# Kernel optimization log

Hardware: AMD Instinct MI355X
Metric: run time of the kernel (lower is better)

Reference implementation:

```python
import jax, jax.numpy as jnp
import numpy as np

N, E, D, H, G, C = 50000, 600000, 128, 128, 512, 1000
HP = H // 5  # attention-MLP bottleneck (hidden_dim // 5)


def setup_inputs() -> dict:
    key = jax.random.key(0)
    ks = jax.random.split(key, 18)
    cfg_nodes = jax.random.normal(ks[0], (N, D), jnp.float32)
    cfg_relations = jax.random.randint(ks[1], (2, E), 0, N, dtype=jnp.int32)
    pos = jnp.sort(jax.random.randint(ks[2], (G + 1,), 0, N, dtype=jnp.int32))
    node_pos = pos.at[0].set(0).at[-1].set(N)

    def lin(k, fi, fo):
        return jax.random.normal(k, (fi, fo), jnp.float32) / np.sqrt(fi)

    return dict(
        cfg_nodes=cfg_nodes, cfg_relations=cfg_relations, node_pos=node_pos,
        # GATConv layer 1 (in=D, out=H, heads=1)
        W_g1=lin(ks[3], D, H),
        att_src1=jax.random.normal(ks[4], (H,), jnp.float32) / np.sqrt(H),
        att_dst1=jax.random.normal(ks[5], (H,), jnp.float32) / np.sqrt(H),
        b_g1=jnp.zeros((H,), jnp.float32),
        # GATConv layer 2 (in=H, out=H, heads=1, concat=False)
        W_g2=lin(ks[6], H, H),
        att_src2=jax.random.normal(ks[7], (H,), jnp.float32) / np.sqrt(H),
        att_dst2=jax.random.normal(ks[8], (H,), jnp.float32) / np.sqrt(H),
        b_g2=jnp.zeros((H,), jnp.float32),
        # GraphLocalAttention projection MLP
        Wp1=lin(ks[9], H, HP), bp1=jnp.zeros((HP,), jnp.float32),
        Wp2=jax.random.normal(ks[10], (HP,), jnp.float32) / np.sqrt(HP),
        bp2=jnp.zeros((), jnp.float32),
        # final classifier
        Wl=lin(ks[11], H, C), bl=jnp.zeros((C,), jnp.float32),
    )


def _gat_conv(x, src, dst, W, a_src, a_dst, b, n_nodes):
    # PyG GATConv (heads=1): h = xW; e_ij = LeakyReLU(a_s.h_j + a_d.h_i);
    # alpha = softmax over incoming edges of each target; out_i = sum alpha*h_j + b
    h = x @ W                                    # [N, F]
    as_ = h @ a_src                              # [N]
    ad_ = h @ a_dst                              # [N]
    e = jax.nn.leaky_relu(as_[src] + ad_[dst], 0.2)   # [E]
    m = jax.ops.segment_max(e, dst, num_segments=n_nodes)
    ex = jnp.exp(e - m[dst])
    s = jax.ops.segment_sum(ex, dst, num_segments=n_nodes)
    alpha = ex / s[dst]
    out = jax.ops.segment_sum(alpha[:, None] * h[src], dst, num_segments=n_nodes)
    return out + b


def reference(cfg_nodes, cfg_relations, node_pos,
              W_g1, att_src1, att_dst1, b_g1,
              W_g2, att_src2, att_dst2, b_g2,
              Wp1, bp1, Wp2, bp2, Wl, bl):
    n = cfg_nodes.shape[0]
    # add self-loops (PyG GATConv default)
    loops = jnp.arange(n, dtype=cfg_relations.dtype)
    src = jnp.concatenate([cfg_relations[0], loops])
    dst = jnp.concatenate([cfg_relations[1], loops])
    # dropout layers are identity in eval mode
    x = _gat_conv(cfg_nodes, src, dst, W_g1, att_src1, att_dst1, b_g1, n)
    x = jax.nn.elu(x)
    x = _gat_conv(x, src, dst, W_g2, att_src2, att_dst2, b_g2, n)
    # ragged segment attention pooling (attn_by_batch, fully vectorized)
    energy = jax.nn.relu(x @ Wp1 + bp1) @ Wp2 + bp2          # [N]
    seg = jnp.clip(jnp.searchsorted(node_pos, jnp.arange(n), side='right') - 1, 0, G - 1)
    m = jax.ops.segment_max(energy, seg, num_segments=G)
    ex = jnp.exp(energy - m[seg])
    s = jax.ops.segment_sum(ex, seg, num_segments=G)
    w = ex / s[seg]                                           # per-segment softmax
    pooled = jax.ops.segment_sum(w[:, None] * x, seg, num_segments=G)  # [G, H]
    return pooled @ Wl + bl                                   # [G, C]
```

## Files before the change

kernel.cpp:

```cpp
#include <hip/hip_runtime.h>
#include <hip/hip_bf16.h>
#include <math.h>

#define WAVE 64
#define GR 32

typedef __attribute__((ext_vector_type(8))) _Float16 half8;
typedef __attribute__((ext_vector_type(4))) float f32x4;
typedef __attribute__((ext_vector_type(4))) _Float16 half4;

__global__ void count_pack(const int* __restrict__ dst, int* __restrict__ deg, int E, int nbC,
                           const float* __restrict__ W1, const float* __restrict__ W2,
                           _Float16* __restrict__ W1h, _Float16* __restrict__ W2h,
                           const float* __restrict__ Wp1, int HP,
                           _Float16* __restrict__ Ph) {
    int b = blockIdx.x;
    if (b < nbC) {
        int e = (b * 256 + threadIdx.x) * 2;
        if (e + 1 < E) {
            int2 d = *(const int2*)(dst + e);
            atomicAdd(&deg[d.x], 1);
            atomicAdd(&deg[d.y], 1);
        } else if (e < E) {
            atomicAdd(&deg[dst[e]], 1);
        }
    } else if (b < nbC + 128) {
        int pb = b - nbC;
        const float* W = (pb >= 64) ? W2 : W1;
        _Float16* Hf = (pb >= 64) ? W2h : W1h;
        int idx = (pb & 63) * 256 + threadIdx.x;
        int j = idx & 7;
        int lane = (idx >> 3) & 63;
        int kc = (idx >> 9) & 3;
        int nt = idx >> 11;
        int k = kc * 32 + (lane >> 4) * 8 + j;
        int ncol = nt * 16 + (lane & 15);
        Hf[idx] = (_Float16)W[k * 128 + ncol];
    } else {
        int idx = (b - nbC - 128) * 256 + threadIdx.x;
        int j = idx & 7;
        int lane = (idx >> 3) & 63;
        int kc = (idx >> 9) & 3;
        int nt = idx >> 11;
        int k = kc * 32 + (lane >> 4) * 8 + j;
        int ncol = nt * 16 + (lane & 15);
        float x = (ncol < HP) ? Wp1[k * HP + ncol] : 0.f;
        Ph[idx] = (_Float16)x;
    }
}

__global__ void scan_block(const int* __restrict__ in, int* __restrict__ part,
                           int* __restrict__ bsums, int n) {
    __shared__ int tmp[256];
    int tid = threadIdx.x;
    int i = blockIdx.x * 256 + tid;
    int v = (i < n) ? in[i] : 0;
    tmp[tid] = v;
    __syncthreads();
    for (int o = 1; o < 256; o <<= 1) {
        int t = (tid >= o) ? tmp[tid - o] : 0;
        __syncthreads();
        tmp[tid] += t;
        __syncthreads();
    }
    if (i < n) part[i] = tmp[tid] - v;
    if (tid == 255) bsums[blockIdx.x] = tmp[255];
}

__global__ void scan_finish(const int* __restrict__ part, const int* __restrict__ bsums,
                            int* __restrict__ offs, int* __restrict__ cursor,
                            int n, int Etot) {
    __shared__ int acc[256];
    int b = blockIdx.x, tid = threadIdx.x;
    int s = 0;
    for (int i = tid; i < b; i += 256) s += bsums[i];
    acc[tid] = s;
    __syncthreads();
    for (int o = 128; o > 0; o >>= 1) {
        if (tid < o) acc[tid] += acc[tid + o];
        __syncthreads();
    }
    int prefix = acc[0];
    int i = b * 256 + tid;
    if (i < n) {
        int v = part[i] + prefix;
        offs[i] = v;
        cursor[i] = v;
    }
    if (b == 0 && tid == 0) offs[n] = Etot;
}

__global__ void scatter_edges(const int* __restrict__ src, const int* __restrict__ dst,
                              int* __restrict__ cursor, int* __restrict__ csr_src,
                              int* __restrict__ csr_dst, int E) {
    int e = (blockIdx.x * 256 + threadIdx.x) * 2;
    if (e + 1 < E) {
        int2 d = *(const int2*)(dst + e);
        int2 s = *(const int2*)(src + e);
        int p0 = atomicAdd(&cursor[d.x], 1);
        csr_src[p0] = s.x;
        csr_dst[p0] = d.x;
        int p1 = atomicAdd(&cursor[d.y], 1);
        csr_src[p1] = s.y;
        csr_dst[p1] = d.y;
    } else if (e < E) {
        int p = atomicAdd(&cursor[dst[e]], 1);
        csr_src[p] = src[e];
        csr_dst[p] = dst[e];
    }
}

__global__ __launch_bounds__(256) void gemm_mfma(const float* __restrict__ X,
                                                 const _Float16* __restrict__ Bh,
                                                 const float* __restrict__ a_s,
                                                 const float* __restrict__ a_d,
                                                 _Float16* __restrict__ Hout,
                                                 float* __restrict__ as_,
                                                 float* __restrict__ ad_, int n) {
    __shared__ char lds[GR * 136 * 4];
    _Float16* Xh = (_Float16*)lds;
    float* Hs = (float*)lds;

    int tid = threadIdx.x;
    int base = blockIdx.x * GR;
    const float4* X4 = (const float4*)X;

#pragma unroll
    for (int i = 0; i < 4; ++i) {
        int idx = i * 256 + tid;
        int row = idx >> 5, c4 = idx & 31;
        int rs = base + row; if (rs >= n) rs = n - 1;
        float4 v = X4[(size_t)rs * 32 + c4];
        half4 hv = {(_Float16)v.x, (_Float16)v.y, (_Float16)v.z, (_Float16)v.w};
        *(half4*)(Xh + row * 136 + c4 * 4) = hv;
    }
    __syncthreads();

    int wid = tid >> 6, lane = tid & 63;
    int quad = lane >> 4, l16 = lane & 15;
    int rowA = (wid & 1) * 16 + l16;
    int ntb = (wid >> 1) * 4;

    f32x4 acc[4];
#pragma unroll
    for (int t = 0; t < 4; ++t) acc[t] = (f32x4){0.f, 0.f, 0.f, 0.f};

    for (int kc = 0; kc < 4; ++kc) {
        half8 Ah = *(const half8*)(Xh + rowA * 136 + kc * 32 + quad * 8);
#pragma unroll
        for (int nt = 0; nt < 4; ++nt) {
            half8 Bv = *(const half8*)(Bh + (((size_t)((ntb + nt) * 4 + kc)) * 64 + lane) * 8);
            acc[nt] = __builtin_amdgcn_mfma_f32_16x16x32_f16(Ah, Bv, acc[nt], 0, 0, 0);
        }
    }
    __syncthreads();

    int rowD0 = (wid & 1) * 16 + quad * 4;
#pragma unroll
    for (int nt = 0; nt < 4; ++nt)
#pragma unroll
        for (int r = 0; r < 4; ++r)
            Hs[(rowD0 + r) * 136 + (ntb + nt) * 16 + l16] = acc[nt][r];
    __syncthreads();

    const float4* Hs4 = (const float4*)Hs;
    half4* H4 = (half4*)Hout;
#pragma unroll
    for (int i = 0; i < 4; ++i) {
        int idx = i * 256 + tid;
        int row = idx >> 5, c4 = idx & 31;
        int grow = base + row;
        if (grow < n) {
            float4 v = Hs4[row * 34 + c4];
            half4 hv = {(_Float16)v.x, (_Float16)v.y, (_Float16)v.z, (_Float16)v.w};
            H4[(size_t)grow * 32 + c4] = hv;
        }
    }

    int drow = tid >> 3, q = tid & 7;
    const float4* as4 = (const float4*)a_s;
    const float4* ad4 = (const float4*)a_d;
    float s = 0.f, d = 0.f;
#pragma unroll
    for (int j = 0; j < 4; ++j) {
        float4 v = Hs4[drow * 34 + q * 4 + j];
        float4 a = as4[q * 4 + j];
        float4 b = ad4[q * 4 + j];
        s += v.x * a.x + v.y * a.y + v.z * a.z + v.w * a.w;
        d += v.x * b.x + v.y * b.y + v.z * b.z + v.w * b.w;
    }
    s += __shfl_xor(s, 1, WAVE); s += __shfl_xor(s, 2, WAVE); s += __shfl_xor(s, 4, WAVE);
    d += __shfl_xor(d, 1, WAVE); d += __shfl_xor(d, 2, WAVE); d += __shfl_xor(d, 4, WAVE);
    if (q == 0 && base + drow < n) {
        as_[base + drow] = s;
        ad_[base + drow] = d;
    }
}

__device__ __forceinline__ float leaky02(float x) { return x > 0.f ? x : 0.2f * x; }

__global__ __launch_bounds__(256) void edge_weights(const int* __restrict__ csr_src,
                                                    const int* __restrict__ csr_dst,
                                                    const float* __restrict__ as_,
                                                    const float* __restrict__ ad_,
                                                    int2* __restrict__ sw, int E) {
    int i = (blockIdx.x * 256 + threadIdx.x) * 4;
    if (i + 3 < E) {
        int4 s = *(const int4*)(csr_src + i);
        int4 d = *(const int4*)(csr_dst + i);
        float wx = __expf(leaky02(as_[s.x] + ad_[d.x]));
        float wy = __expf(leaky02(as_[s.y] + ad_[d.y]));
        float wz = __expf(leaky02(as_[s.z] + ad_[d.z]));
        float ww = __expf(leaky02(as_[s.w] + ad_[d.w]));
        int4 lo = make_int4(s.x, __float_as_int(wx), s.y, __float_as_int(wy));
        int4 hi = make_int4(s.z, __float_as_int(wz), s.w, __float_as_int(ww));
        *(int4*)(sw + i) = lo;
        *(int4*)(sw + i + 2) = hi;
    } else {
        for (; i < E; ++i) {
            float w = __expf(leaky02(as_[csr_src[i]] + ad_[csr_dst[i]]));
            sw[i] = make_int2(csr_src[i], __float_as_int(w));
        }
    }
}

__global__ __launch_bounds__(256) void gat_aggregate(const _Float16* __restrict__ h,
                                                     const int2* __restrict__ sw,
                                                     const float* __restrict__ as_,
                                                     const float* __restrict__ ad_,
                                                     const int* __restrict__ offs,
                                                     const float* __restrict__ bias,
                                                     float* __restrict__ out, int n, int act) {
    int node = blockIdx.x * 4 + (threadIdx.x >> 6);
    int lane = threadIdx.x & 63;
    if (node >= n) return;
    int beg = offs[node], end = offs[node + 1];
    int q4 = lane >> 4, l = lane & 15;
    const half8* h8 = (const half8*)h;

    float w_self = __expf(leaky02(as_[node] + ad_[node]));
    float facc[8];
    {
        half8 v = h8[(size_t)node * 16 + l];
        float ws = (q4 == 0) ? w_self : 0.f;
#pragma unroll
        for (int i = 0; i < 8; ++i) facc[i] = ws * (float)v[i];
    }
    float sacc = (lane == 0) ? w_self : 0.f;
#pragma unroll 2
    for (int j = beg; j < end; j += 4) {
        int j0 = j + q4;
        bool valid = j0 < end;
        int jc = valid ? j0 : (end - 1);
        int2 e = sw[jc];
        int s = valid ? e.x : node;
        float w = valid ? __int_as_float(e.y) : 0.f;
        half8 v = h8[(size_t)s * 16 + l];
#pragma unroll
        for (int i = 0; i < 8; ++i) facc[i] = fmaf(w, (float)v[i], facc[i]);
        sacc += (l == 0) ? w : 0.f;
    }
#pragma unroll
    for (int i = 0; i < 8; ++i) {
        facc[i] += __shfl_xor(facc[i], 16, WAVE);
        facc[i] += __shfl_xor(facc[i], 32, WAVE);
    }
    sacc += __shfl_xor(sacc, 16, WAVE);
    sacc += __shfl_xor(sacc, 32, WAVE);
    float inv_s = 1.f / __shfl(sacc, 0, WAVE);
    if (q4 == 0) {
        const float4* b4 = (const float4*)bias;
        float4 b0 = b4[l * 2], b1 = b4[l * 2 + 1];
        float4 o0, o1;
        o0.x = fmaf(facc[0], inv_s, b0.x);
        o0.y = fmaf(facc[1], inv_s, b0.y);
        o0.z = fmaf(facc[2], inv_s, b0.z);
        o0.w = fmaf(facc[3], inv_s, b0.w);
        o1.x = fmaf(facc[4], inv_s, b1.x);
        o1.y = fmaf(facc[5], inv_s, b1.y);
        o1.z = fmaf(facc[6], inv_s, b1.z);
        o1.w = fmaf(facc[7], inv_s, b1.w);
        if (act == 1) {
            o0.x = o0.x > 0.f ? o0.x : expm1f(o0.x);
            o0.y = o0.y > 0.f ? o0.y : expm1f(o0.y);
            o0.z = o0.z > 0.f ? o0.z : expm1f(o0.z);
            o0.w = o0.w > 0.f ? o0.w : expm1f(o0.w);
            o1.x = o1.x > 0.f ? o1.x : expm1f(o1.x);
            o1.y = o1.y > 0.f ? o1.y : expm1f(o1.y);
            o1.z = o1.z > 0.f ? o1.z : expm1f(o1.z);
            o1.w = o1.w > 0.f ? o1.w : expm1f(o1.w);
        }
        float4* o4 = (float4*)(out + (size_t)node * 128);
        o4[l * 2] = o0;
        o4[l * 2 + 1] = o1;
    }
}

__global__ __launch_bounds__(256) void energy_mfma(const float* __restrict__ X,
                                                   const _Float16* __restrict__ Ph,
                                                   const float* __restrict__ bp1,
                                                   const float* __restrict__ Wp2,
                                                   const float* __restrict__ bp2,
                                                   float* __restrict__ energy, int n, int HP) {
    __shared__ _Float16 Xh[GR * 136];
    int tid = threadIdx.x;
    int base = blockIdx.x * GR;
    const float4* X4 = (const float4*)X;
#pragma unroll
    for (int i = 0; i < 4; ++i) {
        int idx = i * 256 + tid;
        int row = idx >> 5, c4 = idx & 31;
        int rs = base + row; if (rs >= n) rs = n - 1;
        float4 v = X4[(size_t)rs * 32 + c4];
        half4 hv = {(_Float16)v.x, (_Float16)v.y, (_Float16)v.z, (_Float16)v.w};
        *(half4*)(Xh + row * 136 + c4 * 4) = hv;
    }
    __syncthreads();

    int wid = tid >> 6, lane = tid & 63;
    if (wid >= 2) return;
    int quad = lane >> 4, l16 = lane & 15;
    int rowA = wid * 16 + l16;

    f32x4 acc0 = (f32x4){0.f, 0.f, 0.f, 0.f};
    f32x4 acc1 = (f32x4){0.f, 0.f, 0.f, 0.f};
    for (int kc = 0; kc < 4; ++kc) {
        half8 Ah = *(const half8*)(Xh + rowA * 136 + kc * 32 + quad * 8);
        half8 B0 = *(const half8*)(Ph + (((size_t)kc) * 64 + lane) * 8);
        half8 B1 = *(const half8*)(Ph + (((size_t)(4 + kc)) * 64 + lane) * 8);
        acc0 = __builtin_amdgcn_mfma_f32_16x16x32_f16(Ah, B0, acc0, 0, 0, 0);
        acc1 = __builtin_amdgcn_mfma_f32_16x16x32_f16(Ah, B1, acc1, 0, 0, 0);
    }

    float b0 = bp1[l16];
    float w0 = Wp2[l16];
    int c1 = 16 + l16;
    int c1c = c1 < HP ? c1 : HP - 1;
    float b1 = bp1[c1c];
    float w1 = (c1 < HP) ? Wp2[c1c] : 0.f;
    float bp2v = bp2[0];
#pragma unroll
    for (int r = 0; r < 4; ++r) {
        float h0 = acc0[r] + b0;
        h0 = h0 > 0.f ? h0 : 0.f;
        float h1 = acc1[r] + b1;
        h1 = h1 > 0.f ? h1 : 0.f;
        float v = h0 * w0 + h1 * w1;
        v += __shfl_xor(v, 1, WAVE);
        v += __shfl_xor(v, 2, WAVE);
        v += __shfl_xor(v, 4, WAVE);
        v += __shfl_xor(v, 8, WAVE);
        int row = base + wid * 16 + quad * 4 + r;
        if (l16 == 0 && row < n) energy[row] = v + bp2v;
    }
}

__global__ __launch_bounds__(256) void seg_pool_classify(const float* __restrict__ X,
                                                         const float* __restrict__ energy,
                                                         const int* __restrict__ node_pos,
                                                         const float* __restrict__ Wl,
                                                         const float* __restrict__ bl,
                                                         float* __restrict__ out, int C) {
    int g = blockIdx.x;
    int beg = node_pos[g], end = node_pos[g + 1];
    int tid = threadIdx.x;
    __shared__ float sred[256];
    __shared__ float4 red[256];
    __shared__ float pP[128];

    float m = -INFINITY;
    for (int i = beg + tid; i < end; i += 256) m = fmaxf(m, energy[i]);
    sred[tid] = m;
    __syncthreads();
    for (int o = 128; o > 0; o >>= 1) {
        if (tid < o) sred[tid] = fmaxf(sred[tid], sred[tid + o]);
        __syncthreads();
    }
    m = sred[0];
    __syncthreads();
    float s = 0.f;
    for (int i = beg + tid; i < end; i += 256) s += __expf(energy[i] - m);
    sred[tid] = s;
    __syncthreads();
    for (int o = 128; o > 0; o >>= 1) {
        if (tid < o) sred[tid] += sred[tid + o];
        __syncthreads();
    }
    s = sred[0];
    __syncthreads();
    float inv = (end > beg && s > 0.f) ? 1.f / s : 0.f;

    int quad = tid & 31;
    int rg = tid >> 5;
    const float4* X4 = (const float4*)X;
    float4 acc = make_float4(0.f, 0.f, 0.f, 0.f);
    for (int i = beg + rg; i < end; i += 8) {
        float w = __expf(energy[i] - m) * inv;
        float4 v = X4[(size_t)i * 32 + quad];
        acc.x = fmaf(w, v.x, acc.x);
        acc.y = fmaf(w, v.y, acc.y);
        acc.z = fmaf(w, v.z, acc.z);
        acc.w = fmaf(w, v.w, acc.w);
    }
    red[tid] = acc;
    __syncthreads();
    if (rg < 4) {
        float4 o = red[tid + 128];
        acc.x += o.x; acc.y += o.y; acc.z += o.z; acc.w += o.w;
        red[tid] = acc;
    }
    __syncthreads();
    if (rg < 2) {
        float4 o = red[tid + 64];
        acc.x += o.x; acc.y += o.y; acc.z += o.z; acc.w += o.w;
        red[tid] = acc;
    }
    __syncthreads();
    if (rg == 0) {
        float4 o = red[tid + 32];
        acc.x += o.x; acc.y += o.y; acc.z += o.z; acc.w += o.w;
        pP[4 * quad + 0] = acc.x;
        pP[4 * quad + 1] = acc.y;
        pP[4 * quad + 2] = acc.z;
        pP[4 * quad + 3] = acc.w;
    }
    __syncthreads();

    for (int c = tid; c < C; c += 256) {
        float a = bl[c];
#pragma unroll 8
        for (int k = 0; k < 128; ++k) a = fmaf(pP[k], Wl[(size_t)k * C + c], a);
        out[(size_t)g * C + c] = a;
    }
}

extern "C" void kernel_launch(void* const* d_in, const int* in_sizes, int n_in,
                              void* d_out, int out_size, void* d_ws, size_t ws_size,
                              hipStream_t stream) {
    const float* cfg_nodes = (const float*)d_in[0];
    const int* rel = (const int*)d_in[1];
    const int* node_pos = (const int*)d_in[2];
    const float* W_g1 = (const float*)d_in[3];
    const float* att_src1 = (const float*)d_in[4];
    const float* att_dst1 = (const float*)d_in[5];
    const float* b_g1 = (const float*)d_in[6];
    const float* W_g2 = (const float*)d_in[7];
    const float* att_src2 = (const float*)d_in[8];
    const float* att_dst2 = (const float*)d_in[9];
    const float* b_g2 = (const float*)d_in[10];
    const float* Wp1 = (const float*)d_in[11];
    const float* bp1 = (const float*)d_in[12];
    const float* Wp2 = (const float*)d_in[13];
    const float* bp2 = (const float*)d_in[14];
    const float* Wl = (const float*)d_in[15];
    const float* bl = (const float*)d_in[16];

    const int N = in_sizes[0] / 128;
    const int E = in_sizes[1] / 2;
    const int G = in_sizes[2] - 1;
    const int HP = in_sizes[12];
    const int C = out_size / G;

    const int* srcArr = rel;
    const int* dstArr = rel + E;

    char* w = (char*)d_ws;
    auto carve = [&](size_t bytes) -> char* {
        char* p = w;
        w += (bytes + 255) & ~(size_t)255;
        return p;
    };
    _Float16* bufH = (_Float16*)carve((size_t)N * 128 * 2);
    float* bufB = (float*)carve((size_t)N * 128 * 4);
    float* asv = (float*)carve((size_t)N * 4);
    float* adv = (float*)carve((size_t)N * 4);
    float* energy = (float*)carve((size_t)N * 4);
    int* deg = (int*)carve((size_t)N * 4);
    int* offs = (int*)carve((size_t)(N + 1) * 4);
    int* cursor = (int*)carve((size_t)N * 4);
    int* csr_src = (int*)carve((size_t)E * 4);
    int* csr_dst = (int*)carve((size_t)E * 4);
    int2* swbuf = (int2*)carve((size_t)E * 8);
    int* bsums = (int*)carve(1024);
    _Float16* W1h = (_Float16*)carve(16384 * 2);
    _Float16* W2h = (_Float16*)carve(16384 * 2);
    _Float16* Ph = (_Float16*)carve(4096 * 2);

    const int nbN = (N + 255) / 256;
    const int nbC = ((E + 1) / 2 + 255) / 256;
    const int nbT = (N + GR - 1) / GR;
    const int nbW = (E + 1023) / 1024;

    hipMemsetAsync(deg, 0, (size_t)N * 4, stream);
    count_pack<<<nbC + 144, 256, 0, stream>>>(dstArr, deg, E, nbC,
                                              W_g1, W_g2, W1h, W2h, Wp1, HP, Ph);
    scan_block<<<nbN, 256, 0, stream>>>(deg, offs, bsums, N);
    scan_finish<<<nbN, 256, 0, stream>>>(offs, bsums, offs, cursor, N, E);
    scatter_edges<<<nbC, 256, 0, stream>>>(srcArr, dstArr, cursor, csr_src, csr_dst, E);

    gemm_mfma<<<nbT, 256, 0, stream>>>(cfg_nodes, W1h, att_src1, att_dst1,
                                       bufH, asv, adv, N);
    edge_weights<<<nbW, 256, 0, stream>>>(csr_src, csr_dst, asv, adv, swbuf, E);
    gat_aggregate<<<(N + 3) / 4, 256, 0, stream>>>(bufH, swbuf, asv, adv, offs, b_g1, bufB, N, 1);

    gemm_mfma<<<nbT, 256, 0, stream>>>(bufB, W2h, att_src2, att_dst2,
                                       bufH, asv, adv, N);
    edge_weights<<<nbW, 256, 0, stream>>>(csr_src, csr_dst, asv, adv, swbuf, E);
    gat_aggregate<<<(N + 3) / 4, 256, 0, stream>>>(bufH, swbuf, asv, adv, offs, b_g2, bufB, N, 0);

    energy_mfma<<<nbT, 256, 0, stream>>>(bufB, Ph, bp1, Wp2, bp2, energy, N, HP);
    seg_pool_classify<<<G, 256, 0, stream>>>(bufB, energy, node_pos, Wl, bl, (float*)d_out, C);
}
```

Before: 315.2 us.

## Split pooling from classifier and run classifier as batched MFMA GEMM

The fused per-segment pool+classify kernel is split into a pooling kernel that writes pooled [G,128] rows and a separate fp16 MFMA GEMM for pooled @ Wl. Wl is pre-packed into an MFMA-friendly fp16 layout by a new kernel. The old classifier had every one of the 512 blocks stream all of Wl (128x1000) with scalar FMAs, and the GEMM now shares each Wl tile across 32 segments. Block reductions also move from shared-memory trees to wave shuffles. The change costs two extra launches and an fp16 rounding of the pooled activations and Wl.

```diff
diff --git a/kernel.cpp b/kernel.cpp
--- a/kernel.cpp
+++ b/kernel.cpp
@@ -47,6 +47,18 @@
         float x = (ncol < HP) ? Wp1[k * HP + ncol] : 0.f;
         Ph[idx] = (_Float16)x;
     }
+}
+
+__global__ void pack_wl(const float* __restrict__ Wl, int C, _Float16* __restrict__ Wlh) {
+    int idx = blockIdx.x * 256 + threadIdx.x;
+    int j = idx & 7;
+    int lane = (idx >> 3) & 63;
+    int kc = (idx >> 9) & 3;
+    int nt = idx >> 11;
+    int k = kc * 32 + (lane >> 4) * 8 + j;
+    int ncol = nt * 16 + (lane & 15);
+    float x = (ncol < C) ? Wl[(size_t)k * C + ncol] : 0.f;
+    Wlh[idx] = (_Float16)x;
 }
 
 __global__ void scan_block(const int* __restrict__ in, int* __restrict__ part,
@@ -355,45 +367,39 @@
     }
 }
 
-__global__ __launch_bounds__(256) void seg_pool_classify(const float* __restrict__ X,
-                                                         const float* __restrict__ energy,
-                                                         const int* __restrict__ node_pos,
-                                                         const float* __restrict__ Wl,
-                                                         const float* __restrict__ bl,
-                                                         float* __restrict__ out, int C) {
+__global__ __launch_bounds__(256) void seg_pool(const float* __restrict__ X,
+                                                const float* __restrict__ energy,
+                                                const int* __restrict__ node_pos,
+                                                float* __restrict__ pooled) {
     int g = blockIdx.x;
     int beg = node_pos[g], end = node_pos[g + 1];
     int tid = threadIdx.x;
-    __shared__ float sred[256];
+    int wid = tid >> 6, lane = tid & 63;
+    __shared__ float swr[8];
     __shared__ float4 red[256];
-    __shared__ float pP[128];
 
     float m = -INFINITY;
     for (int i = beg + tid; i < end; i += 256) m = fmaxf(m, energy[i]);
-    sred[tid] = m;
-    __syncthreads();
-    for (int o = 128; o > 0; o >>= 1) {
-        if (tid < o) sred[tid] = fmaxf(sred[tid], sred[tid + o]);
-        __syncthreads();
-    }
-    m = sred[0];
-    __syncthreads();
+#pragma unroll
+    for (int o = 1; o < 64; o <<= 1) m = fmaxf(m, __shfl_xor(m, o, WAVE));
+    if (lane == 0) swr[wid] = m;
+    __syncthreads();
+    m = fmaxf(fmaxf(swr[0], swr[1]), fmaxf(swr[2], swr[3]));
+
     float s = 0.f;
     for (int i = beg + tid; i < end; i += 256) s += __expf(energy[i] - m);
-    sred[tid] = s;
-    __syncthreads();
-    for (int o = 128; o > 0; o >>= 1) {
-        if (tid < o) sred[tid] += sred[tid + o];
-        __syncthreads();
-    }
-    s = sred[0];
-    __syncthreads();
+#pragma unroll
+    for (int o = 1; o < 64; o <<= 1) s += __shfl_xor(s, o, WAVE);
+    if (lane == 0) swr[4 + wid] = s;
+    __syncthreads();
+    s = swr[4] + swr[5] + swr[6] + swr[7];
     float inv = (end > beg && s > 0.f) ? 1.f / s : 0.f;
 
     int quad = tid & 31;
     int rg = tid >> 5;
     const float4* X4 = (const float4*)X;
     float4 acc = make_float4(0.f, 0.f, 0.f, 0.f);
+#pragma unroll 2
     for (int i = beg + rg; i < end; i += 8) {
         float w = __expf(energy[i] - m) * inv;
         float4 v = X4[(size_t)i * 32 + quad];
@@ -419,18 +425,62 @@
     if (rg == 0) {
         float4 o = red[tid + 32];
         acc.x += o.x; acc.y += o.y; acc.z += o.z; acc.w += o.w;
-        pP[4 * quad + 0] = acc.x;
-        pP[4 * quad + 1] = acc.y;
-        pP[4 * quad + 2] = acc.z;
-        pP[4 * quad + 3] = acc.w;
-    }
-    __syncthreads();
-
-    for (int c = tid; c < C; c += 256) {
-        float a = bl[c];
-#pragma unroll 8
-        for (int k = 0; k < 128; ++k) a = fmaf(pP[k], Wl[(size_t)k * C + c], a);
-        out[(size_t)g * C + c] = a;
+        ((float4*)(pooled + (size_t)g * 128))[quad] = acc;
+    }
+}
+
+__global__ __launch_bounds__(256) void classify_mfma(const float* __restrict__ P,
+                                                     const _Float16* __restrict__ Wlh,
+                                                     const float* __restrict__ bl,
+                                                     float* __restrict__ out,
+                                                     int G_, int C, int nbM) {
+    __shared__ _Float16 Xh[GR * 136];
+    int tid = threadIdx.x;
+    int bm = blockIdx.x % nbM;
+    int bn = blockIdx.x / nbM;
+    int base = bm * GR;
+    const float4* X4 = (const float4*)P;
+#pragma unroll
+    for (int i = 0; i < 4; ++i) {
+        int idx = i * 256 + tid;
+        int row = idx >> 5, c4 = idx & 31;
+        int rs = base + row; if (rs >= G_) rs = G_ - 1;
+        float4 v = X4[(size_t)rs * 32 + c4];
+        half4 hv = {(_Float16)v.x, (_Float16)v.y, (_Float16)v.z, (_Float16)v.w};
+        *(half4*)(Xh + row * 136 + c4 * 4) = hv;
+    }
+    __syncthreads();
+
+    int wid = tid >> 6, lane = tid & 63;
+    int quad = lane >> 4, l16 = lane & 15;
+    int rowA = (wid & 1) * 16 + l16;
+    int ntb = bn * 8 + (wid >> 1) * 4;
+
+    f32x4 acc[4];
+#pragma unroll
+    for (int t = 0; t < 4; ++t) acc[t] = (f32x4){0.f, 0.f, 0.f, 0.f};
+
+    for (int kc = 0; kc < 4; ++kc) {
+        half8 Ah = *(const half8*)(Xh + rowA * 136 + kc * 32 + quad * 8);
+#pragma unroll
+        for (int nt = 0; nt < 4; ++nt) {
+            half8 Bv = *(const half8*)(Wlh + (((size_t)((ntb + nt) * 4 + kc)) * 64 + lane) * 8);
+            acc[nt] = __builtin_amdgcn_mfma_f32_16x16x32_f16(Ah, Bv, acc[nt], 0, 0, 0);
+        }
+    }
+
+    int row0 = base + (wid & 1) * 16 + quad * 4;
+#pragma unroll
+    for (int nt = 0; nt < 4; ++nt) {
+        int col = (ntb + nt) * 16 + l16;
+        if (col < C) {
+            float b = bl[col];
+#pragma unroll
+            for (int r = 0; r < 4; ++r) {
+                int row = row0 + r;
+                if (row < G_) out[(size_t)row * C + col] = acc[nt][r] + b;
+            }
+        }
     }
 }
 
@@ -485,15 +535,20 @@
     _Float16* W1h = (_Float16*)carve(16384 * 2);
     _Float16* W2h = (_Float16*)carve(16384 * 2);
     _Float16* Ph = (_Float16*)carve(4096 * 2);
+    _Float16* Wlh = (_Float16*)carve(131072 * 2);
+    float* pooled = (float*)carve((size_t)G * 128 * 4);
 
     const int nbN = (N + 255) / 256;
     const int nbC = ((E + 1) / 2 + 255) / 256;
     const int nbT = (N + GR - 1) / GR;
     const int nbW = (E + 1023) / 1024;
+    const int nbM = (G + GR - 1) / GR;
+    const int nbCt = (C + 127) / 128;
 
     hipMemsetAsync(deg, 0, (size_t)N * 4, stream);
     count_pack<<<nbC + 144, 256, 0, stream>>>(dstArr, deg, E, nbC,
                                               W_g1, W_g2, W1h, W2h, Wp1, HP, Ph);
+    pack_wl<<<512, 256, 0, stream>>>(Wl, C, Wlh);
     scan_block<<<nbN, 256, 0, stream>>>(deg, offs, bsums, N);
     scan_finish<<<nbN, 256, 0, stream>>>(offs, bsums, offs, cursor, N, E);
     scatter_edges<<<nbC, 256, 0, stream>>>(srcArr, dstArr, cursor, csr_src, csr_dst, E);
@@ -509,5 +564,6 @@
     gat_aggregate<<<(N + 3) / 4, 256, 0, stream>>>(bufH, swbuf, asv, adv, offs, b_g2, bufB, N, 0);
 
     energy_mfma<<<nbT, 256, 0, stream>>>(bufB, Ph, bp1, Wp2, bp2, energy, N, HP);
-    seg_pool_classify<<<G, 256, 0, stream>>>(bufB, energy, node_pos, Wl, bl, (float*)d_out, C);
-}
+    seg_pool<<<G, 256, 0, stream>>>(bufB, energy, node_pos, pooled);
+    classify_mfma<<<nbM * nbCt, 256, 0, stream>>>(pooled, Wlh, bl, (float*)d_out, G, C, nbM);
+}
```

New measurement: 304.8 us. 1.03x faster.
